# Performance work log

Hardware: AMD Instinct MI355X
Metric: run time of the kernel (lower is better)

The kernel has to match this reference:

```python
import jax, jax.numpy as jnp
import numpy as np
import math

K = 1.0          # Lorentz manifold curvature param: points satisfy <x,x>_L = -K
NUM_HEADS = 16
EPS = 1e-6
B, L, D = 2, 2048, 1024


def lorentz_inner(x, y):
    # <x,y>_L = -x0*y0 + sum_{i>0} xi*yi  (over last dim)
    return jnp.sum(x * y, axis=-1) - 2.0 * x[..., 0] * y[..., 0]


def project_to_lorentz(z):
    # treat z[...,1:] as space components, recompute time so <x,x>_L = -K
    space = z[..., 1:]
    time = jnp.sqrt(K + jnp.sum(space * space, axis=-1, keepdims=True))
    return jnp.concatenate([time, space], axis=-1)


def hlinear(x, W, b, num_heads):
    # Lorentz linear layer (Chen et al. 2022): Euclidean affine map on the
    # ambient coordinates followed by curvature-aware time re-normalization.
    z = x @ W.T + b  # (B, L, D)
    if num_heads > 0:
        Bz, Lz, Dz = z.shape
        z = z.reshape(Bz, Lz, num_heads, Dz // num_heads)  # (B, L, H, dh)
    return project_to_lorentz(z)


def setup_inputs() -> dict:
    key = jax.random.key(0)
    ks = jax.random.split(key, 8)
    def mk_point(k):
        # random manifold points: random space part, valid time coordinate
        z = jax.random.normal(k, (B, L, D), dtype=jnp.float32) * 0.5
        return project_to_lorentz(z)
    scale = 1.0 / math.sqrt(D)
    def mk_w(k):
        return jax.random.normal(k, (D, D), dtype=jnp.float32) * scale
    return {
        "query": mk_point(ks[0]),
        "key": mk_point(ks[1]),
        "value": mk_point(ks[2]),
        "W_Q": mk_w(ks[3]), "b_Q": jnp.zeros((D,), jnp.float32),
        "W_K": mk_w(ks[4]), "b_K": jnp.zeros((D,), jnp.float32),
        "W_V": mk_w(ks[5]), "b_V": jnp.zeros((D,), jnp.float32),
        "W_O": mk_w(ks[6]), "b_O": jnp.zeros((D,), jnp.float32),
    }


def reference(query, key, value, W_Q, b_Q, W_K, b_K, W_V, b_V, W_O, b_O):
    H = NUM_HEADS
    q = hlinear(query, W_Q, b_Q, H)  # (B, L, H, dh) on per-head Lorentz manifold
    k = hlinear(key, W_K, b_K, H)
    v = hlinear(value, W_V, b_V, H)
    dh = q.shape[-1]
    # Lorentzian inner products <q_i, k_j>_L per head: (B, H, Lq, Lk)
    ip = (jnp.einsum('bqhd,bkhd->bhqk', q, k)
          - 2.0 * jnp.einsum('bqh,bkh->bhqk', q[..., 0], k[..., 0]))
    # negative squared Lorentz distance: -d_L^2 = 2K + 2<q,k>_L, scaled by sqrt(dh)
    scores = (2.0 * K + 2.0 * ip) * (1.0 / math.sqrt(dh))
    attn = jax.nn.softmax(scores, axis=-1)
    # Lorentzian centroid aggregation (Law et al.): normalize weighted sum back
    # onto the hyperboloid.
    mu = jnp.einsum('bhqk,bkhd->bqhd', attn, v)  # (B, L, H, dh)
    norm = jnp.sqrt(jnp.maximum(jnp.abs(lorentz_inner(mu, mu)), EPS))
    out_heads = math.sqrt(K) * mu / norm[..., None]
    cat = out_heads.reshape(out_heads.shape[0], out_heads.shape[1], -1)  # (B, L, D)
    return hlinear(cat, W_O, b_O, 0)  # (B, L, D) on the manifold
```

## Files before the change

### kernel.cpp

```cpp
#include <hip/hip_runtime.h>
#include <math.h>

namespace {
constexpr int Ln = 2048;
constexpr int Dn = 1024;
constexpr int Mn = 4096;
constexpr float QSCALE = 0.25f * 1.44269504088896340736f;
}

typedef unsigned short u16;
typedef unsigned int u32;
typedef __attribute__((ext_vector_type(4))) float f32x4;
typedef __attribute__((ext_vector_type(8))) __bf16 bf16x8;
typedef __attribute__((ext_vector_type(4))) unsigned short u16x4;
typedef __attribute__((ext_vector_type(8))) unsigned short u16x8;
typedef __attribute__((ext_vector_type(4))) unsigned int u32x4;


__device__ __forceinline__ u16 f2bf(float f) {
    union { float f; unsigned u; } cv; cv.f = f;
    unsigned u = cv.u + 0x7fffu + ((cv.u >> 16) & 1u);
    return (u16)(u >> 16);
}
__device__ __forceinline__ float bf2f(u16 h) {
    union { unsigned u; float f; } cv; cv.u = ((unsigned)h) << 16;
    return cv.f;
}

__device__ __forceinline__ u32 pkbf(float a, float b) {
    union { __bf16 h[2]; u32 u; } cv;
    cv.h[0] = (__bf16)a; cv.h[1] = (__bf16)b;
    return cv.u;
}

#if __has_builtin(__builtin_amdgcn_exp2f)
__device__ __forceinline__ float exp2_fast(float x) {
    return __builtin_amdgcn_exp2f(x);
}
#else
__device__ __forceinline__ float exp2_fast(float x) {
    float r;
    asm("v_exp_f32 %0, %1" : "=v"(r) : "v"(x));
    return r;
}
#endif

template <int CTRL>
__device__ __forceinline__ float dppf(float x) {
    return __int_as_float(__builtin_amdgcn_update_dpp(
        0, __float_as_int(x), CTRL, 0xf, 0xf, true));
}
__device__ __forceinline__ float red16_add(float x) {
    x += dppf<0xB1>(x);
    x += dppf<0x4E>(x);
    x += dppf<0x141>(x);
    x += dppf<0x140>(x);
    return x;
}

__device__ __forceinline__ void gload16(const void* g, void* l) {
    __builtin_amdgcn_global_load_lds(
        (const __attribute__((address_space(1))) unsigned int*)g,
        (__attribute__((address_space(3))) unsigned int*)l, 16, 0, 0);
}

__global__ __launch_bounds__(256)
void cvt_in3(const float* __restrict__ i0, const float* __restrict__ i1,
             const float* __restrict__ i2,
             u16* __restrict__ o0, u16* __restrict__ o1, u16* __restrict__ o2)
{
    const int z = blockIdx.y;
    const float* in = z == 0 ? i0 : (z == 1 ? i1 : i2);
    u16* out       = z == 0 ? o0 : (z == 1 ? o1 : o2);
    int i = blockIdx.x * 256 + threadIdx.x;
    f32x4 v = ((const f32x4*)in)[i];
    u16x4 o;
#pragma unroll
    for (int j = 0; j < 4; ++j) o[j] = f2bf(v[j]);
    int l = i >> 8;
    int e = (i & 255) * 4;
    int idx = l * 1024 + (e & ~63) + (((((e >> 3) & 7) ^ (l & 7))) << 3) + (e & 7);
    *(u16x4*)&out[idx] = o;
}

__global__ __launch_bounds__(256)
void cvt_w(const float* __restrict__ w0, const float* __restrict__ w1,
           const float* __restrict__ w2, const float* __restrict__ w3,
           u16* __restrict__ q0, u16* __restrict__ q1,
           u16* __restrict__ q2, u16* __restrict__ q3)
{
    const int z = blockIdx.y;
    int i = blockIdx.x * 256 + threadIdx.x;
    if (z < 3) {
        const float* in = z == 0 ? w0 : (z == 1 ? w1 : w2);
        u16* out       = z == 0 ? q0 : (z == 1 ? q1 : q2);
        f32x4 v = ((const f32x4*)in)[i];
        u16x4 o;
#pragma unroll
        for (int j = 0; j < 4; ++j) o[j] = f2bf(v[j]);
        int l = i >> 8;
        int e = (i & 255) * 4;
        int idx = l * 1024 + (e & ~63) + (((((e >> 3) & 7) ^ (l & 7))) << 3) + (e & 7);
        *(u16x4*)&out[idx] = o;
    } else {
        int o  = i >> 8;
        int s0 = (i & 255) * 4;
        int h = s0 >> 6, sl = s0 & 63, a = sl >> 2;
        const float* src = w3 + (size_t)o * 1024 + h * 64;
        u16x4 ov = { f2bf(src[a]), f2bf(src[16 + a]),
                     f2bf(src[32 + a]), f2bf(src[48 + a]) };
        int idx = o * 1024 + h * 64 + (((sl >> 3) ^ (o & 7)) << 3) + (sl & 7);
        *(u16x4*)&q3[idx] = ov;
    }
}

__global__ __launch_bounds__(256)
void gemm_qkv(const u16* __restrict__ xq, const u16* __restrict__ xk,
              const u16* __restrict__ xv, const u16* __restrict__ wq,
              const u16* __restrict__ wk, const u16* __restrict__ wv,
              const float* __restrict__ bq, const float* __restrict__ bk,
              const float* __restrict__ bv,
              u16* __restrict__ oq, u16* __restrict__ ok, u16* __restrict__ ov)
{
    __shared__ u16 As[2][128 * 64];
    __shared__ u16 Bs[2][128 * 64];
    const int t = threadIdx.x;
    const int lane = t & 63, w = t >> 6;
    const int g = lane >> 4, c = lane & 15;
    const int wr = w >> 1, wc = w & 1;
    const int id = blockIdx.x;
    const int bm = ((id & 7) * 4 + ((id >> 3) & 3)) * 128;
    const int bn = ((id >> 5) & 7) * 128;
    const int z  = id >> 8;

    const u16* A = z == 0 ? xq : (z == 1 ? xk : xv);
    const u16* W = z == 0 ? wq : (z == 1 ? wk : wv);
    const float* bias = z == 0 ? bq : (z == 1 ? bk : bv);
    u16* Ct = z == 0 ? oq : (z == 1 ? ok : ov);
    const float scale = z == 0 ? QSCALE : 1.f;
    const float tsign = z == 0 ? -1.f : 1.f;

    f32x4 acc[4][4];
    const f32x4 z4 = {0.f, 0.f, 0.f, 0.f};
#pragma unroll
    for (int i = 0; i < 4; ++i)
#pragma unroll
        for (int j = 0; j < 4; ++j) acc[i][j] = z4;

    const int sr = t >> 3, sb2 = (t & 7) * 8;
    const u16* Ap = A + (size_t)(bm + sr) * Dn + sb2;
    const u16* Wp = W + (size_t)(bn + sr) * Dn + sb2;

    auto stage = [&](int buf, int k0) {
#pragma unroll
        for (int p = 0; p < 4; ++p) {
            gload16(Ap + (size_t)(p * 32) * Dn + k0, &As[buf][(p * 256 + t) * 8]);
            gload16(Wp + (size_t)(p * 32) * Dn + k0, &Bs[buf][(p * 256 + t) * 8]);
        }
    };

    stage(0, 0);
    for (int ki = 0; ki < 16; ++ki) {
        __syncthreads();
        if (ki + 1 < 16) stage((ki + 1) & 1, (ki + 1) * 64);
        const u16* as = As[ki & 1];
        const u16* bs = Bs[ki & 1];
#pragma unroll
        for (int kk = 0; kk < 2; ++kk) {
            const int so = ((kk * 4 + g) ^ (c & 7)) << 3;
            bf16x8 a[4], b[4];
#pragma unroll
            for (int mi = 0; mi < 4; ++mi)
                a[mi] = *(const bf16x8*)&as[(wr * 64 + mi * 16 + c) * 64 + so];
#pragma unroll
            for (int ni = 0; ni < 4; ++ni)
                b[ni] = *(const bf16x8*)&bs[(wc * 64 + ni * 16 + c) * 64 + so];
            __builtin_amdgcn_s_setprio(1);
#pragma unroll
            for (int mi = 0; mi < 4; ++mi)
#pragma unroll
                for (int ni = 0; ni < 4; ++ni)
                    acc[mi][ni] = __builtin_amdgcn_mfma_f32_16x16x32_bf16(
                        a[mi], b[ni], acc[mi][ni], 0, 0, 0);
            __builtin_amdgcn_s_setprio(0);
        }
    }

    const int hcb = bn + wc * 64;
    const int h = hcb >> 6;
#pragma unroll
    for (int mi = 0; mi < 4; ++mi)
#pragma unroll
        for (int j = 0; j < 4; ++j) {
            int ll = bm + wr * 64 + mi * 16 + g * 4 + j;
            float zv[4];
#pragma unroll
            for (int ni = 0; ni < 4; ++ni)
                zv[ni] = acc[mi][ni][j] + bias[hcb + ni * 16 + c];
            float loc = zv[0]*zv[0] + zv[1]*zv[1] + zv[2]*zv[2] + zv[3]*zv[3];
            if (c == 0) loc -= zv[0] * zv[0];
            loc = red16_add(loc);
            float tval = sqrtf(1.f + loc);
            float v0 = (c == 0) ? tsign * tval : zv[0];
            int bb = ll >> 11, l2 = ll & 2047;
            u16* dst = Ct + (((size_t)bb * 16 + h) * Ln + l2) * 64;
            u16x4 pkv = { f2bf(v0 * scale), f2bf(zv[1] * scale),
                          f2bf(zv[2] * scale), f2bf(zv[3] * scale) };
            *(u16x4*)&dst[(4 * c) ^ ((ll & 7) << 3)] = pkv;
        }
}

__global__ __launch_bounds__(256)
void transpose_v(const u16* __restrict__ vin, u16* __restrict__ vout)
{
    __shared__ u16 raw[64 * 64];
    const int t = threadIdx.x;
    const int bh = blockIdx.x, lc = blockIdx.y;
    const u16* src = vin + ((size_t)bh * Ln + lc * 64) * 64;
#pragma unroll
    for (int p = 0; p < 2; ++p) {
        int ci = p * 256 + t;
        *(u16x8*)&raw[ci * 8] = *(const u16x8*)(src + ci * 8);
    }
    __syncthreads();
    const int d = t >> 2, cp0 = (t & 3) * 16;
    const int s = ((d & 15) << 2) | (d >> 4);
    u16 buf[16];
#pragma unroll
    for (int i = 0; i < 16; ++i) {
        int cp = cp0 + i;
        int n = ((cp >> 5) << 5) | (((cp >> 2) & 1) << 4) | (((cp >> 3) & 3) << 2) | (cp & 3);
        buf[i] = raw[n * 64 + ((((s >> 3) ^ (n & 7)) << 3) | (s & 7))];
    }
    u16* dst = vout + ((size_t)bh * 64 + d) * Ln + lc * 64;
    int b0 = cp0 >> 3;
    *(u16x8*)&dst[((b0 ^ (d & 7)) << 3)]       = *(const u16x8*)&buf[0];
    *(u16x8*)&dst[(((b0 + 1) ^ (d & 7)) << 3)] = *(const u16x8*)&buf[8];
}

__global__ __launch_bounds__(256, 4)
void attn_mfma(const u16* __restrict__ qt, const u16* __restrict__ kt,
               const u16* __restrict__ vT, u16* __restrict__ part)
{
    __shared__ u16 smem[4 * 4096];

    const int t = threadIdx.x;
    const int lane = t & 63, w = t >> 6;
    const int g = lane >> 4, c = lane & 15;
    const int id  = blockIdx.x;
    const int qb  = (id >> 3) & 15;
    const int gidx = (id & 7) | ((id >> 7) << 3);
    const int bh  = gidx & 31;
    const int kvh = gidx >> 5;
    const int q0  = qb * 128;
    const u16* Q = qt + (size_t)bh * Ln * 64;
    const u16* K = kt + (size_t)bh * Ln * 64 + (size_t)kvh * (1024 * 64);
    const u16* V = vT + (size_t)bh * 64 * (size_t)Ln + kvh * 1024;

    bf16x8 qa[2][2];
#pragma unroll
    for (int mi = 0; mi < 2; ++mi)
#pragma unroll
        for (int kk = 0; kk < 2; ++kk) {
            int row = q0 + w * 32 + mi * 16 + c;
            qa[mi][kk] = *(const bf16x8*)(Q + (size_t)row * 64 +
                                          (((kk * 4 + g) ^ (c & 7)) << 3));
        }

    f32x4 o[2][4];
    const f32x4 z4 = {0.f, 0.f, 0.f, 0.f};
#pragma unroll
    for (int mi = 0; mi < 2; ++mi)
#pragma unroll
        for (int di = 0; di < 4; ++di) o[mi][di] = z4;

    const int fb0 = c * 128 + (((0 + g) ^ (c & 7)) << 4);
    const int fb1 = c * 128 + (((4 + g) ^ (c & 7)) << 4);

    char* sb = (char*)smem;
    const int cr = t >> 3, cb = t & 7;
    const u16* kp = K + (size_t)cr * 64 + cb * 8;
    const u16* vp = V + (size_t)cr * Ln + cb * 8;

    gload16(kp,            sb + t * 16);
    gload16(kp + 2048,     sb + 4096 + t * 16);
    gload16(vp,            sb + 16384 + t * 16);
    gload16(vp + 32 * Ln,  sb + 16384 + 4096 + t * 16);

    constexpr int NC = 1024 / 64;
    for (int ch = 0; ch < NC; ++ch) {
        __syncthreads();
        if (ch + 1 < NC) {
            const u16* kn = kp + (ch + 1) * 4096;
            const u16* vn = vp + (ch + 1) * 64;
            char* db = sb + (((ch + 1) & 1) << 13);
            gload16(kn,           db + t * 16);
            gload16(kn + 2048,    db + 4096 + t * 16);
            gload16(vn,           db + 16384 + t * 16);
            gload16(vn + 32 * Ln, db + 16384 + 4096 + t * 16);
        }
        const char* kbb = sb + ((ch & 1) << 13);
        const char* vbb = kbb + 16384;

        f32x4 sf[2][4];
#pragma unroll
        for (int mi = 0; mi < 2; ++mi)
#pragma unroll
            for (int ni = 0; ni < 4; ++ni) sf[mi][ni] = z4;
        __builtin_amdgcn_s_setprio(1);
#pragma unroll
        for (int kk = 0; kk < 2; ++kk) {
            const int fb = kk ? fb1 : fb0;
            bf16x8 kb[4];
#pragma unroll
            for (int ni = 0; ni < 4; ++ni)
                kb[ni] = *(const bf16x8*)(kbb + fb + ni * 2048);
#pragma unroll
            for (int mi = 0; mi < 2; ++mi)
#pragma unroll
                for (int ni = 0; ni < 4; ++ni)
                    sf[mi][ni] = __builtin_amdgcn_mfma_f32_16x16x32_bf16(
                        kb[ni], qa[mi][kk], sf[mi][ni], 0, 0, 0);
        }
        __builtin_amdgcn_s_setprio(0);

        bf16x8 paf[2][2];
#pragma unroll
        for (int mi = 0; mi < 2; ++mi) {
            float ex[4][4];
#pragma unroll
            for (int ni = 0; ni < 4; ++ni)
#pragma unroll
                for (int j = 0; j < 4; ++j)
                    ex[ni][j] = exp2_fast(sf[mi][ni][j]);
            u32x4 p0 = { pkbf(ex[0][0], ex[0][1]), pkbf(ex[0][2], ex[0][3]),
                         pkbf(ex[1][0], ex[1][1]), pkbf(ex[1][2], ex[1][3]) };
            u32x4 p1 = { pkbf(ex[2][0], ex[2][1]), pkbf(ex[2][2], ex[2][3]),
                         pkbf(ex[3][0], ex[3][1]), pkbf(ex[3][2], ex[3][3]) };
            paf[mi][0] = __builtin_bit_cast(bf16x8, p0);
            paf[mi][1] = __builtin_bit_cast(bf16x8, p1);
        }

        __builtin_amdgcn_s_setprio(1);
#pragma unroll
        for (int kk = 0; kk < 2; ++kk) {
            const int fb = kk ? fb1 : fb0;
#pragma unroll
            for (int di = 0; di < 4; ++di) {
                bf16x8 vb = *(const bf16x8*)(vbb + fb + di * 2048);
#pragma unroll
                for (int mi = 0; mi < 2; ++mi)
                    o[mi][di] = __builtin_amdgcn_mfma_f32_16x16x32_bf16(
                        paf[mi][kk], vb, o[mi][di], 0, 0, 0);
            }
        }
        __builtin_amdgcn_s_setprio(0);
    }

    u16* P = part + (size_t)(kvh * 32 + bh) * (4 * 2048 * 16);
#pragma unroll
    for (int mi = 0; mi < 2; ++mi)
#pragma unroll
        for (int j = 0; j < 4; ++j) {
            int row = q0 + w * 32 + mi * 16 + g * 4 + j;
#pragma unroll
            for (int di = 0; di < 4; ++di)
                P[(di * 2048 + row) * 16 + c] = f2bf(o[mi][di][j]);
        }
}

__global__ __launch_bounds__(256)
void attn_combine(const u16* __restrict__ part, u16* __restrict__ cat)
{
    const int grp = blockIdx.x * 16 + (threadIdx.x >> 4);
    const int c = threadIdx.x & 15;
    const int bh = grp >> 11, q = grp & 2047;
    const u16* P0 = part + (size_t)bh * (4 * 2048 * 16);
    const u16* P1 = part + (size_t)(32 + bh) * (4 * 2048 * 16);
    float mu[4];
#pragma unroll
    for (int di = 0; di < 4; ++di) {
        int idx = (di * 2048 + q) * 16 + c;
        mu[di] = bf2f(P0[idx]) + bf2f(P1[idx]);
    }
    float loc = mu[0]*mu[0] + mu[1]*mu[1] + mu[2]*mu[2] + mu[3]*mu[3];
    if (c == 0) loc -= 2.f * mu[0] * mu[0];
    loc = red16_add(loc);
    float rn = rsqrtf(fmaxf(fabsf(loc), 1e-6f));
    const int b = bh >> 4, h = bh & 15;
    u16* dst = cat + ((size_t)b * Ln + q) * Dn + h * 64;
    u16x4 pkv = { f2bf(mu[0] * rn), f2bf(mu[1] * rn),
                  f2bf(mu[2] * rn), f2bf(mu[3] * rn) };
    *(u16x4*)&dst[(4 * c) ^ ((q & 7) << 3)] = pkv;
}

__global__ __launch_bounds__(256)
void gemm_o(const u16* __restrict__ A, const u16* __restrict__ B,
            const float* __restrict__ bias, float* __restrict__ C)
{
    __shared__ u16 As[2][64 * 64];
    __shared__ u16 Bs[2][128 * 64];
    const int t = threadIdx.x;
    const int lane = t & 63, w = t >> 6;
    const int g = lane >> 4, c = lane & 15;
    const int wr = w >> 1, wc = w & 1;
    const int id = blockIdx.x;
    const int bm = ((id & 7) * 8 + ((id >> 3) & 7)) * 64;
    const int bn = (id >> 6) * 128;

    f32x4 acc[2][4];
    const f32x4 z4 = {0.f, 0.f, 0.f, 0.f};
#pragma unroll
    for (int i = 0; i < 2; ++i)
#pragma unroll
        for (int j = 0; j < 4; ++j) acc[i][j] = z4;

    const int sr = t >> 3, sb2 = (t & 7) * 8;
    const u16* Ap = A + (size_t)(bm + sr) * Dn + sb2;
    const u16* Bp = B + (size_t)(bn + sr) * Dn + sb2;

    auto stage = [&](int buf, int k0) {
        gload16(Ap + k0,            &As[buf][t * 8]);
        gload16(Ap + 32 * Dn + k0,  &As[buf][(256 + t) * 8]);
        gload16(Bp + k0,            &Bs[buf][t * 8]);
        gload16(Bp + 32 * Dn + k0,  &Bs[buf][(256 + t) * 8]);
        gload16(Bp + 64 * Dn + k0,  &Bs[buf][(512 + t) * 8]);
        gload16(Bp + 96 * Dn + k0,  &Bs[buf][(768 + t) * 8]);
    };

    stage(0, 0);
    for (int ki = 0; ki < 16; ++ki) {
        __syncthreads();
        if (ki + 1 < 16) stage((ki + 1) & 1, (ki + 1) * 64);
        const u16* as = As[ki & 1];
        const u16* bs = Bs[ki & 1];
#pragma unroll
        for (int kk = 0; kk < 2; ++kk) {
            const int so = ((kk * 4 + g) ^ (c & 7)) << 3;
            bf16x8 a[2], b[4];
#pragma unroll
            for (int mi = 0; mi < 2; ++mi)
                a[mi] = *(const bf16x8*)&as[(wr * 32 + mi * 16 + c) * 64 + so];
#pragma unroll
            for (int ni = 0; ni < 4; ++ni)
                b[ni] = *(const bf16x8*)&bs[(wc * 64 + ni * 16 + c) * 64 + so];
            __builtin_amdgcn_s_setprio(1);
#pragma unroll
            for (int mi = 0; mi < 2; ++mi)
#pragma unroll
                for (int ni = 0; ni < 4; ++ni)
                    acc[mi][ni] = __builtin_amdgcn_mfma_f32_16x16x32_bf16(
                        a[mi], b[ni], acc[mi][ni], 0, 0, 0);
            __builtin_amdgcn_s_setprio(0);
        }
    }

#pragma unroll
    for (int mi = 0; mi < 2; ++mi)
#pragma unroll
        for (int j = 0; j < 4; ++j) {
            size_t row = bm + wr * 32 + mi * 16 + g * 4 + j;
#pragma unroll
            for (int ni = 0; ni < 4; ++ni) {
                int col = bn + wc * 64 + ni * 16 + c;
                C[row * Dn + col] = acc[mi][ni][j] + bias[col];
            }
        }
}

__global__ __launch_bounds__(256)
void lorentz_row_full(float* __restrict__ z)
{
    __shared__ float red[4];
    const int t = threadIdx.x;
    const size_t base = (size_t)blockIdx.x * Dn;
    float4 v = *(const float4*)&z[base + t * 4];
    if (t == 0) v.x = 0.f;
    float ssq = v.x * v.x + v.y * v.y + v.z * v.z + v.w * v.w;
#pragma unroll
    for (int off = 32; off; off >>= 1) ssq += __shfl_xor(ssq, off);
    if ((t & 63) == 0) red[t >> 6] = ssq;
    __syncthreads();
    if (t == 0) z[base] = sqrtf(1.0f + red[0] + red[1] + red[2] + red[3]);
}

extern "C" void kernel_launch(void* const* d_in, const int* in_sizes, int n_in,
                              void* d_out, int out_size, void* d_ws, size_t ws_size,
                              hipStream_t stream)
{
    const float* query = (const float*)d_in[0];
    const float* key_  = (const float*)d_in[1];
    const float* value = (const float*)d_in[2];
    const float* W_Q   = (const float*)d_in[3];
    const float* b_Q   = (const float*)d_in[4];
    const float* W_K   = (const float*)d_in[5];
    const float* b_K   = (const float*)d_in[6];
    const float* W_V   = (const float*)d_in[7];
    const float* b_V   = (const float*)d_in[8];
    const float* W_O   = (const float*)d_in[9];
    const float* b_O   = (const float*)d_in[10];

    const size_t MD = (size_t)Mn * Dn;
    const size_t DD = (size_t)Dn * Dn;
    u16* xq   = (u16*)d_ws;
    u16* xk   = xq + MD;
    u16* xv   = xk + MD;
    u16* wo   = xv + MD;
    u16* q_t  = wo + DD;
    u16* k_t  = q_t + MD;
    u16* wq   = k_t + MD;
    u16* wk   = wq + DD;
    u16* wv   = wk + DD;
    u16* v_ln = wv + DD;
    u16* part = wq;
    u16* v_T  = xv;
    u16* cat  = xk;

    dim3 ci(Mn * Dn / 1024, 3);
    cvt_in3<<<ci, 256, 0, stream>>>(query, key_, value, xq, xk, xv);
    dim3 cw(Dn * Dn / 1024, 4);
    cvt_w<<<cw, 256, 0, stream>>>(W_Q, W_K, W_V, W_O, wq, wk, wv, wo);

    gemm_qkv<<<768, 256, 0, stream>>>(xq, xk, xv, wq, wk, wv,
                                      b_Q, b_K, b_V, q_t, k_t, v_ln);

    dim3 tg(32, Ln / 64);
    transpose_v<<<tg, 256, 0, stream>>>(v_ln, v_T);

    attn_mfma<<<1024, 256, 0, stream>>>(q_t, k_t, v_T, part);

    attn_combine<<<4096, 256, 0, stream>>>(part, cat);

    gemm_o<<<512, 256, 0, stream>>>(cat, wo, b_O, (float*)d_out);
    lorentz_row_full<<<Mn, 256, 0, stream>>>((float*)d_out);
}
```

Before: 132.2 us.

## Load QKV GEMM fragments directly from global memory into registers

```diff
diff --git a/kernel.cpp b/kernel.cpp
--- a/kernel.cpp
+++ b/kernel.cpp
@@ -122,14 +122,12 @@
               const float* __restrict__ bv,
               u16* __restrict__ oq, u16* __restrict__ ok, u16* __restrict__ ov)
 {
-    __shared__ u16 As[2][128 * 64];
-    __shared__ u16 Bs[2][128 * 64];
     const int t = threadIdx.x;
     const int lane = t & 63, w = t >> 6;
     const int g = lane >> 4, c = lane & 15;
     const int wr = w >> 1, wc = w & 1;
     const int id = blockIdx.x;
-    const int bm = ((id & 7) * 4 + ((id >> 3) & 3)) * 128;
+    const int bm = (id & 31) * 128;
     const int bn = ((id >> 5) & 7) * 128;
     const int z  = id >> 8;
 
@@ -140,6 +138,18 @@
     const float scale = z == 0 ? QSCALE : 1.f;
     const float tsign = z == 0 ? -1.f : 1.f;
 
+    const int s7 = c & 7;
+    const int ko0 = ((0 + g) ^ s7) << 3;
+    const int ko1 = ((4 + g) ^ s7) << 3;
+    const u16* Ab[4];
+    const u16* Bb[4];
+#pragma unroll
+    for (int mi = 0; mi < 4; ++mi)
+        Ab[mi] = A + (size_t)(bm + wr * 64 + mi * 16 + c) * Dn;
+#pragma unroll
+    for (int ni = 0; ni < 4; ++ni)
+        Bb[ni] = W + (size_t)(bn + wc * 64 + ni * 16 + c) * Dn;
+
     f32x4 acc[4][4];
     const f32x4 z4 = {0.f, 0.f, 0.f, 0.f};
 #pragma unroll
@@ -147,43 +157,42 @@
 #pragma unroll
         for (int j = 0; j < 4; ++j) acc[i][j] = z4;
 
-    const int sr = t >> 3, sb2 = (t & 7) * 8;
-    const u16* Ap = A + (size_t)(bm + sr) * Dn + sb2;
-    const u16* Wp = W + (size_t)(bn + sr) * Dn + sb2;
-
-    auto stage = [&](int buf, int k0) {
-#pragma unroll
-        for (int p = 0; p < 4; ++p) {
-            gload16(Ap + (size_t)(p * 32) * Dn + k0, &As[buf][(p * 256 + t) * 8]);
-            gload16(Wp + (size_t)(p * 32) * Dn + k0, &Bs[buf][(p * 256 + t) * 8]);
-        }
-    };
-
-    stage(0, 0);
+    bf16x8 a0[4], b0[4], a1[4], b1[4];
+#pragma unroll
+    for (int mi = 0; mi < 4; ++mi) a0[mi] = *(const bf16x8*)(Ab[mi] + ko0);
+#pragma unroll
+    for (int ni = 0; ni < 4; ++ni) b0[ni] = *(const bf16x8*)(Bb[ni] + ko0);
+
     for (int ki = 0; ki < 16; ++ki) {
-        __syncthreads();
-        if (ki + 1 < 16) stage((ki + 1) & 1, (ki + 1) * 64);
-        const u16* as = As[ki & 1];
-        const u16* bs = Bs[ki & 1];
-#pragma unroll
-        for (int kk = 0; kk < 2; ++kk) {
-            const int so = ((kk * 4 + g) ^ (c & 7)) << 3;
-            bf16x8 a[4], b[4];
+        const int kb = ki * 64;
+#pragma unroll
+        for (int mi = 0; mi < 4; ++mi) a1[mi] = *(const bf16x8*)(Ab[mi] + kb + ko1);
+#pragma unroll
+        for (int ni = 0; ni < 4; ++ni) b1[ni] = *(const bf16x8*)(Bb[ni] + kb + ko1);
+        __builtin_amdgcn_s_setprio(1);
+#pragma unroll
+        for (int mi = 0; mi < 4; ++mi)
+#pragma unroll
+            for (int ni = 0; ni < 4; ++ni)
+                acc[mi][ni] = __builtin_amdgcn_mfma_f32_16x16x32_bf16(
+                    a0[mi], b0[ni], acc[mi][ni], 0, 0, 0);
+        __builtin_amdgcn_s_setprio(0);
+        if (ki + 1 < 16) {
 #pragma unroll
             for (int mi = 0; mi < 4; ++mi)
-                a[mi] = *(const bf16x8*)&as[(wr * 64 + mi * 16 + c) * 64 + so];
-#pragma unroll
-            for (int ni = 0; ni < 4; ++ni)
-                b[ni] = *(const bf16x8*)&bs[(wc * 64 + ni * 16 + c) * 64 + so];
-            __builtin_amdgcn_s_setprio(1);
-#pragma unroll
-            for (int mi = 0; mi < 4; ++mi)
-#pragma unroll
-                for (int ni = 0; ni < 4; ++ni)
-                    acc[mi][ni] = __builtin_amdgcn_mfma_f32_16x16x32_bf16(
-                        a[mi], b[ni], acc[mi][ni], 0, 0, 0);
-            __builtin_amdgcn_s_setprio(0);
-        }
+                a0[mi] = *(const bf16x8*)(Ab[mi] + kb + 64 + ko0);
+#pragma unroll
+            for (int ni = 0; ni < 4; ++ni)
+                b0[ni] = *(const bf16x8*)(Bb[ni] + kb + 64 + ko0);
+        }
+        __builtin_amdgcn_s_setprio(1);
+#pragma unroll
+        for (int mi = 0; mi < 4; ++mi)
+#pragma unroll
+            for (int ni = 0; ni < 4; ++ni)
+                acc[mi][ni] = __builtin_amdgcn_mfma_f32_16x16x32_bf16(
+                    a1[mi], b1[ni], acc[mi][ni], 0, 0, 0);
+        __builtin_amdgcn_s_setprio(0);
     }
 
     const int hcb = bn + wc * 64;
```

New measurement: 129.2 us (median of 2 runs). -2.3%, faster.
